# Kernel tuning notes

Measured on AMD Instinct MI355X. Metric: run time of the kernel, lower is better.

## Reference

```python
import jax, jax.numpy as jnp
import numpy as np

PI_APPROX = 3.14  # the original module uses 3.14, not math.pi
FPS = 30.0        # hard-coded sampling rate in calc_hr_torch


def setup_inputs() -> dict:
    key = jax.random.key(0)
    x = jax.random.normal(key, (4096, 4096), dtype=jnp.float32)
    return {"x": x}


def reference(x) -> jnp.ndarray:
    test_n, sig_length = x.shape
    # mean-subtract each signal (over last dim)
    x = x - jnp.mean(x, axis=-1, keepdims=True)

    # custom_fft: DFT over dim 0 (size test_n), O(N^2) via trig matmuls
    N = test_n
    n = jnp.arange(N, dtype=jnp.float32)[:, None]  # [N,1]
    k = jnp.arange(N, dtype=jnp.float32)[None, :]  # [1,N]
    ang = (-2.0 * PI_APPROX / N) * (k * n)         # [N,N]
    real_part = jnp.matmul(jnp.cos(ang), x)        # [N, sig_length]
    imag_part = jnp.matmul(jnp.sin(ang), x)

    # custom_rfft: keep non-negative frequencies along dim 0
    half = N // 2 + 1 if N % 2 == 0 else (N + 1) // 2
    real_part = real_part[:half]
    imag_part = imag_part[:half]

    Ns = sig_length
    freq = jnp.arange(Ns, dtype=jnp.float32) / (Ns / FPS)  # [sig_length]
    amplitude = jnp.sqrt(real_part ** 2 + imag_part ** 2) / Ns  # [half, sig_length]
    hr_list = freq[jnp.argmax(amplitude, axis=-1)] * 60.0       # [half]
    return hr_list
```

## Files before the change

### kernel.cpp

```cpp
#include <hip/hip_runtime.h>
#include <cmath>

typedef _Float16 f16;
typedef _Float16 f16x8 __attribute__((ext_vector_type(8)));
typedef float f32x4 __attribute__((ext_vector_type(4)));
typedef unsigned long long u64;

#define M_OUT 2049
#define NDIM 4096
#define MPAD 2112
#define CW ((float)(-2.0 * 3.14 / 4096.0))

static const size_t WS_MEAN  = 0;
static const size_t WS_CELLS = 16384;
static const size_t WS_TBL   = 40960;
static const size_t A_ELEMS  = (size_t)MPAD * NDIM;
static const size_t X_ELEMS  = (size_t)NDIM * NDIM;
static const size_t WS_XTBL  = WS_TBL + 4 * A_ELEMS * sizeof(f16);
static const size_t WS_FULL_END = WS_XTBL + 2 * X_ELEMS * sizeof(f16);
static const size_t WS_MID_END  = WS_TBL + 4 * A_ELEMS * sizeof(f16);

#define AS1 __attribute__((address_space(1)))
#define AS3 __attribute__((address_space(3)))
__device__ __forceinline__ void async_copy16(const void* gsrc, void* ldst) {
    __builtin_amdgcn_global_load_lds((const AS1 unsigned int*)gsrc,
                                     (AS3 unsigned int*)ldst, 16, 0, 0);
}

__device__ __forceinline__ void split_f16(float v, f16& hi, f16& lo) {
    hi = (f16)v;
    lo = (f16)((v - (float)hi) * 64.0f);
}

__global__ void mean_kernel(const float* __restrict__ x, float* __restrict__ meanv,
                            u64* __restrict__ cells) {
    if (blockIdx.x < 9) {
        int i = blockIdx.x * 256 + threadIdx.x;
        if (i < M_OUT) cells[i] = 0ull;
    }
    const int row = blockIdx.x;
    const float4* xr = (const float4*)(x + (size_t)row * NDIM);
    float s = 0.f;
    for (int i = threadIdx.x; i < NDIM / 4; i += 256) {
        float4 v = xr[i];
        s += (v.x + v.y) + (v.z + v.w);
    }
    for (int off = 32; off; off >>= 1) s += __shfl_down(s, off);
    __shared__ float ps[4];
    if ((threadIdx.x & 63) == 0) ps[threadIdx.x >> 6] = s;
    __syncthreads();
    if (threadIdx.x == 0) {
        float t = (ps[0] + ps[1]) + (ps[2] + ps[3]);
        meanv[row] = t * (1.0f / 4096.0f);
    }
}

__global__ __launch_bounds__(256) void nyq_partial(
    const float* __restrict__ x, const float* __restrict__ meanv,
    float* __restrict__ part)
{
    __shared__ float lc[256], ls[256];
    __shared__ float sC[128], sS[128];
    const int t = threadIdx.x;
    const int ks = blockIdx.y;
    const int kbase = ks * 256;
    sincosf(CW * (float)(2048 * (kbase + t)), &ls[t], &lc[t]);
    __syncthreads();
    const int col = blockIdx.x * 128 + (t & 127);
    const int kp  = t >> 7;
    float C = 0.f, S = 0.f;
    const float* xp = x + (size_t)(kbase + kp * 128) * NDIM + col;
    const float* mp = meanv + kbase + kp * 128;
    for (int i = 0; i < 128; ++i) {
        float v = xp[(size_t)i * NDIM] - mp[i];
        C = fmaf(lc[kp * 128 + i], v, C);
        S = fmaf(ls[kp * 128 + i], v, S);
    }
    if (kp) { sC[t - 128] = C; sS[t - 128] = S; }
    __syncthreads();
    if (!kp) {
        part[(size_t)ks * NDIM + col]            = C + sC[t];
        part[(size_t)(16 + ks) * NDIM + col]     = S + sS[t];
    }
}

__global__ __launch_bounds__(256) void nyq_reduce(
    const float* __restrict__ part, u64* __restrict__ cells)
{
    const int n = blockIdx.x * 256 + threadIdx.x;
    float C = 0.f, S = 0.f;
    for (int ks = 0; ks < 16; ++ks) {
        C += part[(size_t)ks * NDIM + n];
        S += part[(size_t)(16 + ks) * NDIM + n];
    }
    float a2 = C * C + S * S;
    u64 key = ((u64)__float_as_uint(a2) << 32) | (unsigned)(~n);
    for (int off = 1; off < 64; off <<= 1) {
        unsigned hi = (unsigned)(key >> 32), lo = (unsigned)key;
        unsigned ho = __shfl_xor(hi, off), lo2 = __shfl_xor(lo, off);
        u64 o = ((u64)ho << 32) | lo2;
        if (o > key) key = o;
    }
    if ((threadIdx.x & 63) == 0) atomicMax(cells + 2048, key);
}

__global__ void fill_tables_cm(const float* __restrict__ x, const float* __restrict__ meanv,
                               f16* __restrict__ atbl, f16* __restrict__ xtbl) {
    const int c = blockIdx.x;
    if (blockIdx.y < 9) {
        const int m = blockIdx.y * 256 + threadIdx.x;
        if (m >= MPAD) return;
        const bool valid = (m < M_OUT);
        f16x8 chv, clv, shv, slv;
        for (int j = 0; j < 8; ++j) {
            float cc = 0.f, ss = 0.f;
            if (valid) {
                int kk = c * 8 + j;
                float ang = CW * (float)(m * kk);
                sincosf(ang, &ss, &cc);
            }
            f16 h, l;
            split_f16(cc, h, l); chv[j] = h; clv[j] = l;
            split_f16(ss, h, l); shv[j] = h; slv[j] = l;
        }
        size_t idx = ((size_t)c * MPAD + m) * 8;
        *(f16x8*)(atbl + idx)                 = chv;
        *(f16x8*)(atbl + A_ELEMS + idx)       = clv;
        *(f16x8*)(atbl + 2 * A_ELEMS + idx)   = shv;
        *(f16x8*)(atbl + 3 * A_ELEMS + idx)   = slv;
    } else {
        const int n = (blockIdx.y - 9) * 256 + threadIdx.x;
        f16x8 hv, lv;
        for (int j = 0; j < 8; ++j) {
            int k = c * 8 + j;
            float v = x[(size_t)k * NDIM + n] - meanv[k];
            f16 h, l;
            split_f16(v, h, l);
            hv[j] = h; lv[j] = l;
        }
        size_t idx = ((size_t)c * NDIM + n) * 8;
        *(f16x8*)(xtbl + idx)           = hv;
        *(f16x8*)(xtbl + X_ELEMS + idx) = lv;
    }
}

__global__ __launch_bounds__(256, 2) void dft_gemm_cm(
    const f16* __restrict__ atbl, const f16* __restrict__ xtbl,
    u64* __restrict__ cells)
{
    __shared__ alignas(16) f16 sX[3][2][4][128][8];

    const int t = threadIdx.x;
    const int n0      = blockIdx.x * 128;
    const int rowBase = blockIdx.y * 64;

    const int lane = t & 63;
    const int w  = t >> 6;
    const int wm = w >> 1, wn = w & 1;
    const int q  = lane >> 4, ln = lane & 15;

    f32x4 aC0[2][4], aC1[2][4], aS0[2][4], aS1[2][4];
#pragma unroll
    for (int i = 0; i < 2; ++i)
#pragma unroll
        for (int j = 0; j < 4; ++j) {
            aC0[i][j] = (f32x4){0.f, 0.f, 0.f, 0.f};
            aC1[i][j] = (f32x4){0.f, 0.f, 0.f, 0.f};
            aS0[i][j] = (f32x4){0.f, 0.f, 0.f, 0.f};
            aS1[i][j] = (f32x4){0.f, 0.f, 0.f, 0.f};
        }

    const f16* aBase = atbl + ((size_t)q * MPAD + (rowBase + wm * 32 + ln)) * 8;

    const int xq0 = w >> 1, xh = w & 1;
    const int xq1 = xq0 + 2;
    const f16* xG0 = xtbl + ((size_t)xq0 * NDIM + n0 + xh * 64 + lane) * 8;
    const f16* xG1 = xtbl + ((size_t)xq1 * NDIM + n0 + xh * 64 + lane) * 8;
    const f16* xG2 = xG0 + X_ELEMS;
    const f16* xG3 = xG1 + X_ELEMS;

    auto loadA = [&](f16x8 (&dst)[2][4], int kc) {
#pragma unroll
        for (int tm = 0; tm < 2; ++tm)
#pragma unroll
            for (int tb = 0; tb < 4; ++tb)
                dst[tm][tb] = *(const f16x8*)(aBase + (size_t)tb * A_ELEMS
                              + ((size_t)kc * MPAD + tm * 16) * 8);
    };

    auto stageX = [&](int buf, int kc) {
        const size_t kadv = (size_t)kc * NDIM * 8;
        async_copy16(xG0 + kadv, &sX[buf][0][xq0][xh * 64][0]);
        async_copy16(xG1 + kadv, &sX[buf][0][xq1][xh * 64][0]);
        async_copy16(xG2 + kadv, &sX[buf][1][xq0][xh * 64][0]);
        async_copy16(xG3 + kadv, &sX[buf][1][xq1][xh * 64][0]);
    };

    auto compute = [&](f16x8 (&A)[2][4], int buf) {
        f16x8 bh[4], bl[4];
#pragma unroll
        for (int tn = 0; tn < 4; ++tn) {
            int nl = wn * 64 + tn * 16 + ln;
            bh[tn] = *(const f16x8*)&sX[buf][0][q][nl][0];
            bl[tn] = *(const f16x8*)&sX[buf][1][q][nl][0];
        }
        __builtin_amdgcn_s_setprio(1);
#pragma unroll
        for (int tm = 0; tm < 2; ++tm)
#pragma unroll
            for (int tn = 0; tn < 4; ++tn) {
                aC0[tm][tn] = __builtin_amdgcn_mfma_f32_16x16x32_f16(A[tm][0], bh[tn], aC0[tm][tn], 0, 0, 0);
                aC1[tm][tn] = __builtin_amdgcn_mfma_f32_16x16x32_f16(A[tm][0], bl[tn], aC1[tm][tn], 0, 0, 0);
                aC1[tm][tn] = __builtin_amdgcn_mfma_f32_16x16x32_f16(A[tm][1], bh[tn], aC1[tm][tn], 0, 0, 0);
                aS0[tm][tn] = __builtin_amdgcn_mfma_f32_16x16x32_f16(A[tm][2], bh[tn], aS0[tm][tn], 0, 0, 0);
                aS1[tm][tn] = __builtin_amdgcn_mfma_f32_16x16x32_f16(A[tm][2], bl[tn], aS1[tm][tn], 0, 0, 0);
                aS1[tm][tn] = __builtin_amdgcn_mfma_f32_16x16x32_f16(A[tm][3], bh[tn], aS1[tm][tn], 0, 0, 0);
            }
        __builtin_amdgcn_s_setprio(0);
    };

    f16x8 Aa[2][4], Ab[2][4];
    int cur = 0, nxt = 1;
    auto bump = [&]() { cur = nxt; nxt = (nxt == 2) ? 0 : nxt + 1; };

    stageX(0, 0);
    loadA(Aa, 0);

    int kc = 0;
    for (int it = 0; it < 63; ++it) {
        loadA(Ab, kc + 4);
        stageX(nxt, kc + 4);
        asm volatile("s_waitcnt vmcnt(12)" ::: "memory");
        __builtin_amdgcn_s_barrier();
        __builtin_amdgcn_sched_barrier(0);
        compute(Aa, cur);
        bump();
        kc += 4;
        loadA(Aa, kc + 4);
        stageX(nxt, kc + 4);
        asm volatile("s_waitcnt vmcnt(12)" ::: "memory");
        __builtin_amdgcn_s_barrier();
        __builtin_amdgcn_sched_barrier(0);
        compute(Ab, cur);
        bump();
        kc += 4;
    }
    loadA(Ab, kc + 4);
    stageX(nxt, kc + 4);
    asm volatile("s_waitcnt vmcnt(12)" ::: "memory");
    __builtin_amdgcn_s_barrier();
    __builtin_amdgcn_sched_barrier(0);
    compute(Aa, cur);
    bump();
    asm volatile("s_waitcnt vmcnt(0)" ::: "memory");
    __builtin_amdgcn_s_barrier();
    __builtin_amdgcn_sched_barrier(0);
    compute(Ab, cur);

    const float inv64 = 0.015625f;
#pragma unroll
    for (int tm = 0; tm < 2; ++tm) {
#pragma unroll
        for (int r = 0; r < 4; ++r) {
            u64 best = 0ull;
#pragma unroll
            for (int tn = 0; tn < 4; ++tn) {
                float C = aC0[tm][tn][r] + aC1[tm][tn][r] * inv64;
                float S = aS0[tm][tn][r] + aS1[tm][tn][r] * inv64;
                float a2 = C * C + S * S;
                int col = n0 + wn * 64 + tn * 16 + ln;
                u64 key = ((u64)__float_as_uint(a2) << 32) | (unsigned)(~col);
                if (key > best) best = key;
            }
            for (int off = 1; off < 16; off <<= 1) {
                unsigned hi = (unsigned)(best >> 32), lo = (unsigned)best;
                unsigned ho = __shfl_xor(hi, off);
                unsigned lo2 = __shfl_xor(lo, off);
                u64 o = ((u64)ho << 32) | lo2;
                if (o > best) best = o;
            }
            if (ln == 0) {
                int grow = rowBase + wm * 32 + tm * 16 + q * 4 + r;
                if (grow < M_OUT) atomicMax(cells + grow, best);
            }
        }
    }
}

__global__ void fill_tables_rm(f16* __restrict__ tbl) {
    long long g = (long long)blockIdx.x * 256 + threadIdx.x;
    if (g >= (long long)(MPAD * 512)) return;
    int m  = (int)(g >> 9);
    int kq = ((int)g & 511) * 8;
    bool valid = (m < M_OUT);
    f16x8 chv, clv, shv, slv;
    for (int j = 0; j < 8; ++j) {
        float c = 0.f, s = 0.f;
        if (valid) {
            int kk = kq + j;
            float ang = CW * (float)(m * kk);
            sincosf(ang, &s, &c);
        }
        f16 h, l;
        split_f16(c, h, l); chv[j] = h; clv[j] = l;
        split_f16(s, h, l); shv[j] = h; slv[j] = l;
    }
    size_t idx = (size_t)m * NDIM + kq;
    *(f16x8*)(tbl + idx)               = chv;
    *(f16x8*)(tbl + A_ELEMS + idx)     = clv;
    *(f16x8*)(tbl + 2 * A_ELEMS + idx) = shv;
    *(f16x8*)(tbl + 3 * A_ELEMS + idx) = slv;
}

#define PK 40
__global__ __launch_bounds__(256, 2) void dft_gemm_fb(
    const float* __restrict__ x, const float* __restrict__ meanv,
    const f16* __restrict__ tbl, int useTbl,
    u64* __restrict__ cells)
{
    __shared__ alignas(16) f16 Ach[64][PK];
    __shared__ alignas(16) f16 Acl[64][PK];
    __shared__ alignas(16) f16 Ash[64][PK];
    __shared__ alignas(16) f16 Asl[64][PK];
    __shared__ alignas(16) f16 Xh[128][PK];
    __shared__ alignas(16) f16 Xl[128][PK];

    const int t = threadIdx.x;
    const int n0      = blockIdx.x * 128;
    const int rowBase = blockIdx.y * 64;

    const int am  = t >> 2;
    const int akq = (t & 3) * 8;
    const int xn  = t & 127;
    const int xkh = (t >> 7) * 16;

    const int lane = t & 63;
    const int w  = t >> 6;
    const int wm = w >> 1, wn = w & 1;
    const int q  = lane >> 4, ln = lane & 15;

    f32x4 aC0[2][4], aC1[2][4], aS0[2][4], aS1[2][4];
    for (int i = 0; i < 2; ++i)
        for (int j = 0; j < 4; ++j) {
            aC0[i][j] = (f32x4){0.f, 0.f, 0.f, 0.f};
            aC1[i][j] = (f32x4){0.f, 0.f, 0.f, 0.f};
            aS0[i][j] = (f32x4){0.f, 0.f, 0.f, 0.f};
            aS1[i][j] = (f32x4){0.f, 0.f, 0.f, 0.f};
        }

    const int arow = rowBase + am;
    const bool avalid = (arow < M_OUT);

    for (int k0 = 0; k0 < NDIM; k0 += 32) {
        __syncthreads();
        if (useTbl) {
            size_t idx = (size_t)arow * NDIM + k0 + akq;
            *(f16x8*)&Ach[am][akq] = *(const f16x8*)(tbl + idx);
            *(f16x8*)&Acl[am][akq] = *(const f16x8*)(tbl + A_ELEMS + idx);
            *(f16x8*)&Ash[am][akq] = *(const f16x8*)(tbl + 2 * A_ELEMS + idx);
            *(f16x8*)&Asl[am][akq] = *(const f16x8*)(tbl + 3 * A_ELEMS + idx);
        } else {
            f16x8 chv, clv, shv, slv;
            for (int j = 0; j < 8; ++j) {
                float c = 0.f, s = 0.f;
                if (avalid) {
                    int kk = k0 + akq + j;
                    float ang = CW * (float)(arow * kk);
                    sincosf(ang, &s, &c);
                }
                f16 h, l;
                split_f16(c, h, l); chv[j] = h; clv[j] = l;
                split_f16(s, h, l); shv[j] = h; slv[j] = l;
            }
            *(f16x8*)&Ach[am][akq] = chv;
            *(f16x8*)&Acl[am][akq] = clv;
            *(f16x8*)&Ash[am][akq] = shv;
            *(f16x8*)&Asl[am][akq] = slv;
        }
        {
            const float* xp = x + (size_t)(k0 + xkh) * NDIM + n0 + xn;
            f16x8 h0, h1, l0, l1;
            for (int r = 0; r < 16; ++r) {
                float v = xp[(size_t)r * NDIM] - meanv[k0 + xkh + r];
                f16 hi, lo;
                split_f16(v, hi, lo);
                if (r < 8) { h0[r] = hi; l0[r] = lo; }
                else       { h1[r - 8] = hi; l1[r - 8] = lo; }
            }
            *(f16x8*)&Xh[xn][xkh]     = h0;
            *(f16x8*)&Xh[xn][xkh + 8] = h1;
            *(f16x8*)&Xl[xn][xkh]     = l0;
            *(f16x8*)&Xl[xn][xkh + 8] = l1;
        }
        __syncthreads();
        f16x8 fch[2], fcl[2], fsh[2], fsl[2], bh[4], bl[4];
        for (int tm = 0; tm < 2; ++tm) {
            int ml = wm * 32 + tm * 16 + ln;
            fch[tm] = *(const f16x8*)&Ach[ml][q * 8];
            fcl[tm] = *(const f16x8*)&Acl[ml][q * 8];
            fsh[tm] = *(const f16x8*)&Ash[ml][q * 8];
            fsl[tm] = *(const f16x8*)&Asl[ml][q * 8];
        }
        for (int tn = 0; tn < 4; ++tn) {
            int nl = wn * 64 + tn * 16 + ln;
            bh[tn] = *(const f16x8*)&Xh[nl][q * 8];
            bl[tn] = *(const f16x8*)&Xl[nl][q * 8];
        }
        for (int tm = 0; tm < 2; ++tm)
            for (int tn = 0; tn < 4; ++tn) {
                aC0[tm][tn] = __builtin_amdgcn_mfma_f32_16x16x32_f16(fch[tm], bh[tn], aC0[tm][tn], 0, 0, 0);
                aC1[tm][tn] = __builtin_amdgcn_mfma_f32_16x16x32_f16(fch[tm], bl[tn], aC1[tm][tn], 0, 0, 0);
                aC1[tm][tn] = __builtin_amdgcn_mfma_f32_16x16x32_f16(fcl[tm], bh[tn], aC1[tm][tn], 0, 0, 0);
                aS0[tm][tn] = __builtin_amdgcn_mfma_f32_16x16x32_f16(fsh[tm], bh[tn], aS0[tm][tn], 0, 0, 0);
                aS1[tm][tn] = __builtin_amdgcn_mfma_f32_16x16x32_f16(fsh[tm], bl[tn], aS1[tm][tn], 0, 0, 0);
                aS1[tm][tn] = __builtin_amdgcn_mfma_f32_16x16x32_f16(fsl[tm], bh[tn], aS1[tm][tn], 0, 0, 0);
            }
    }

    const float inv64 = 0.015625f;
    for (int tm = 0; tm < 2; ++tm) {
        for (int r = 0; r < 4; ++r) {
            u64 best = 0ull;
            for (int tn = 0; tn < 4; ++tn) {
                float C = aC0[tm][tn][r] + aC1[tm][tn][r] * inv64;
                float S = aS0[tm][tn][r] + aS1[tm][tn][r] * inv64;
                float a2 = C * C + S * S;
                int col = n0 + wn * 64 + tn * 16 + ln;
                u64 key = ((u64)__float_as_uint(a2) << 32) | (unsigned)(~col);
                if (key > best) best = key;
            }
            for (int off = 1; off < 16; off <<= 1) {
                unsigned hi = (unsigned)(best >> 32), lo = (unsigned)best;
                unsigned ho = __shfl_xor(hi, off);
                unsigned lo2 = __shfl_xor(lo, off);
                u64 o = ((u64)ho << 32) | lo2;
                if (o > best) best = o;
            }
            if (ln == 0) {
                int grow = rowBase + wm * 32 + tm * 16 + q * 4 + r;
                if (grow < M_OUT) atomicMax(cells + grow, best);
            }
        }
    }
}

__global__ void out_kernel(const u64* __restrict__ cells, float* __restrict__ out) {
    int i = blockIdx.x * 256 + threadIdx.x;
    if (i < M_OUT) {
        unsigned col = ~(unsigned)(cells[i] & 0xFFFFFFFFull);
        float freq = (float)col / (4096.0f / 30.0f);
        out[i] = freq * 60.0f;
    }
}

extern "C" void kernel_launch(void* const* d_in, const int* in_sizes, int n_in,
                              void* d_out, int out_size, void* d_ws, size_t ws_size,
                              hipStream_t stream) {
    const float* x = (const float*)d_in[0];
    char* ws = (char*)d_ws;
    float* meanv = (float*)(ws + WS_MEAN);
    u64*   cells = (u64*)(ws + WS_CELLS);
    f16*   atbl  = (f16*)(ws + WS_TBL);
    f16*   xtbl  = (f16*)(ws + WS_XTBL);
    float* nyqp  = (float*)(ws + WS_TBL);
    float* out   = (float*)d_out;

    hipLaunchKernelGGL(mean_kernel, dim3(NDIM), dim3(256), 0, stream, x, meanv, cells);

    if (ws_size >= WS_FULL_END) {
        hipLaunchKernelGGL(nyq_partial, dim3(32, 16), dim3(256), 0, stream, x, meanv, nyqp);
        hipLaunchKernelGGL(nyq_reduce, dim3(16), dim3(256), 0, stream, nyqp, cells);
        hipLaunchKernelGGL(fill_tables_cm, dim3(512, 25), dim3(256), 0, stream,
                           x, meanv, atbl, xtbl);
        hipLaunchKernelGGL(dft_gemm_cm, dim3(32, 32), dim3(256), 0, stream, atbl, xtbl, cells);
    } else if (ws_size >= WS_MID_END) {
        hipLaunchKernelGGL(fill_tables_rm, dim3(4224), dim3(256), 0, stream, atbl);
        hipLaunchKernelGGL(dft_gemm_fb, dim3(32, 33), dim3(256), 0, stream,
                           x, meanv, atbl, 1, cells);
    } else {
        hipLaunchKernelGGL(dft_gemm_fb, dim3(32, 33), dim3(256), 0, stream,
                           x, meanv, atbl, 0, cells);
    }
    hipLaunchKernelGGL(out_kernel, dim3((M_OUT + 255) / 256), dim3(256), 0, stream, cells, out);
}
```

Before: 458.0 us.

## Merge split-f16 accumulators, drop A double-buffer, raise occupancy to three waves

Stores the low f16 part of each split value unscaled, so the hi and lo MFMA products accumulate into one register set instead of two. This halves the accumulator registers. The A-fragment double buffer is removed and A is loaded just-in-time each k-step, with a tighter vmcnt wait. Launch bounds go up to three blocks per SIMD. Unscaled low parts risk precision loss, since tiny residuals can fall into f16 subnormals, and A loads are now less latency-hidden.

```diff
diff --git a/kernel.cpp b/kernel.cpp
--- a/kernel.cpp
+++ b/kernel.cpp
@@ -30,6 +30,10 @@
 __device__ __forceinline__ void split_f16(float v, f16& hi, f16& lo) {
     hi = (f16)v;
     lo = (f16)((v - (float)hi) * 64.0f);
+}
+__device__ __forceinline__ void split_raw(float v, f16& hi, f16& lo) {
+    hi = (f16)v;
+    lo = (f16)(v - (float)hi);
 }
 
 __global__ void mean_kernel(const float* __restrict__ x, float* __restrict__ meanv,
@@ -120,8 +124,8 @@
                 sincosf(ang, &ss, &cc);
             }
             f16 h, l;
-            split_f16(cc, h, l); chv[j] = h; clv[j] = l;
-            split_f16(ss, h, l); shv[j] = h; slv[j] = l;
+            split_raw(cc, h, l); chv[j] = h; clv[j] = l;
+            split_raw(ss, h, l); shv[j] = h; slv[j] = l;
         }
         size_t idx = ((size_t)c * MPAD + m) * 8;
         *(f16x8*)(atbl + idx)                 = chv;
@@ -135,7 +139,7 @@
             int k = c * 8 + j;
             float v = x[(size_t)k * NDIM + n] - meanv[k];
             f16 h, l;
-            split_f16(v, h, l);
+            split_raw(v, h, l);
             hv[j] = h; lv[j] = l;
         }
         size_t idx = ((size_t)c * NDIM + n) * 8;
@@ -144,7 +148,7 @@
     }
 }
 
-__global__ __launch_bounds__(256, 2) void dft_gemm_cm(
+__global__ __launch_bounds__(256, 3) void dft_gemm_cm(
     const f16* __restrict__ atbl, const f16* __restrict__ xtbl,
     u64* __restrict__ cells)
 {
@@ -159,15 +163,13 @@
     const int wm = w >> 1, wn = w & 1;
     const int q  = lane >> 4, ln = lane & 15;
 
-    f32x4 aC0[2][4], aC1[2][4], aS0[2][4], aS1[2][4];
+    f32x4 aC[2][4], aS[2][4];
 #pragma unroll
     for (int i = 0; i < 2; ++i)
 #pragma unroll
         for (int j = 0; j < 4; ++j) {
-            aC0[i][j] = (f32x4){0.f, 0.f, 0.f, 0.f};
-            aC1[i][j] = (f32x4){0.f, 0.f, 0.f, 0.f};
-            aS0[i][j] = (f32x4){0.f, 0.f, 0.f, 0.f};
-            aS1[i][j] = (f32x4){0.f, 0.f, 0.f, 0.f};
+            aC[i][j] = (f32x4){0.f, 0.f, 0.f, 0.f};
+            aS[i][j] = (f32x4){0.f, 0.f, 0.f, 0.f};
         }
 
     const f16* aBase = atbl + ((size_t)q * MPAD + (rowBase + wm * 32 + ln)) * 8;
@@ -209,55 +211,38 @@
         for (int tm = 0; tm < 2; ++tm)
 #pragma unroll
             for (int tn = 0; tn < 4; ++tn) {
-                aC0[tm][tn] = __builtin_amdgcn_mfma_f32_16x16x32_f16(A[tm][0], bh[tn], aC0[tm][tn], 0, 0, 0);
-                aC1[tm][tn] = __builtin_amdgcn_mfma_f32_16x16x32_f16(A[tm][0], bl[tn], aC1[tm][tn], 0, 0, 0);
-                aC1[tm][tn] = __builtin_amdgcn_mfma_f32_16x16x32_f16(A[tm][1], bh[tn], aC1[tm][tn], 0, 0, 0);
-                aS0[tm][tn] = __builtin_amdgcn_mfma_f32_16x16x32_f16(A[tm][2], bh[tn], aS0[tm][tn], 0, 0, 0);
-                aS1[tm][tn] = __builtin_amdgcn_mfma_f32_16x16x32_f16(A[tm][2], bl[tn], aS1[tm][tn], 0, 0, 0);
-                aS1[tm][tn] = __builtin_amdgcn_mfma_f32_16x16x32_f16(A[tm][3], bh[tn], aS1[tm][tn], 0, 0, 0);
+                aC[tm][tn] = __builtin_amdgcn_mfma_f32_16x16x32_f16(A[tm][0], bh[tn], aC[tm][tn], 0, 0, 0);
+                aC[tm][tn] = __builtin_amdgcn_mfma_f32_16x16x32_f16(A[tm][0], bl[tn], aC[tm][tn], 0, 0, 0);
+                aC[tm][tn] = __builtin_amdgcn_mfma_f32_16x16x32_f16(A[tm][1], bh[tn], aC[tm][tn], 0, 0, 0);
+                aS[tm][tn] = __builtin_amdgcn_mfma_f32_16x16x32_f16(A[tm][2], bh[tn], aS[tm][tn], 0, 0, 0);
+                aS[tm][tn] = __builtin_amdgcn_mfma_f32_16x16x32_f16(A[tm][2], bl[tn], aS[tm][tn], 0, 0, 0);
+                aS[tm][tn] = __builtin_amdgcn_mfma_f32_16x16x32_f16(A[tm][3], bh[tn], aS[tm][tn], 0, 0, 0);
             }
         __builtin_amdgcn_s_setprio(0);
     };
 
-    f16x8 Aa[2][4], Ab[2][4];
+    f16x8 Aa[2][4];
     int cur = 0, nxt = 1;
-    auto bump = [&]() { cur = nxt; nxt = (nxt == 2) ? 0 : nxt + 1; };
 
     stageX(0, 0);
-    loadA(Aa, 0);
-
-    int kc = 0;
-    for (int it = 0; it < 63; ++it) {
-        loadA(Ab, kc + 4);
+
+    for (int kc = 0; kc < 508; kc += 4) {
+        loadA(Aa, kc);
+        __builtin_amdgcn_sched_barrier(0);
         stageX(nxt, kc + 4);
-        asm volatile("s_waitcnt vmcnt(12)" ::: "memory");
+        __builtin_amdgcn_sched_barrier(0);
+        asm volatile("s_waitcnt vmcnt(4)" ::: "memory");
         __builtin_amdgcn_s_barrier();
         __builtin_amdgcn_sched_barrier(0);
         compute(Aa, cur);
-        bump();
-        kc += 4;
-        loadA(Aa, kc + 4);
-        stageX(nxt, kc + 4);
-        asm volatile("s_waitcnt vmcnt(12)" ::: "memory");
-        __builtin_amdgcn_s_barrier();
-        __builtin_amdgcn_sched_barrier(0);
-        compute(Ab, cur);
-        bump();
-        kc += 4;
-    }
-    loadA(Ab, kc + 4);
-    stageX(nxt, kc + 4);
-    asm volatile("s_waitcnt vmcnt(12)" ::: "memory");
+        cur = nxt; nxt = (nxt == 2) ? 0 : nxt + 1;
+    }
+    loadA(Aa, 508);
+    asm volatile("s_waitcnt vmcnt(0)" ::: "memory");
     __builtin_amdgcn_s_barrier();
     __builtin_amdgcn_sched_barrier(0);
     compute(Aa, cur);
-    bump();
-    asm volatile("s_waitcnt vmcnt(0)" ::: "memory");
-    __builtin_amdgcn_s_barrier();
-    __builtin_amdgcn_sched_barrier(0);
-    compute(Ab, cur);
-
-    const float inv64 = 0.015625f;
+
 #pragma unroll
     for (int tm = 0; tm < 2; ++tm) {
 #pragma unroll
@@ -265,8 +250,8 @@
             u64 best = 0ull;
 #pragma unroll
             for (int tn = 0; tn < 4; ++tn) {
-                float C = aC0[tm][tn][r] + aC1[tm][tn][r] * inv64;
-                float S = aS0[tm][tn][r] + aS1[tm][tn][r] * inv64;
+                float C = aC[tm][tn][r];
+                float S = aS[tm][tn][r];
                 float a2 = C * C + S * S;
                 int col = n0 + wn * 64 + tn * 16 + ln;
                 u64 key = ((u64)__float_as_uint(a2) << 32) | (unsigned)(~col);
```

Result: slower. 501.1 us (+9.4%).

## Switch DFT GEMM to 32x32x16 MFMA with unscaled split accumulation

Applied to the files above, without the earlier changes.

Replaces the 16x16x32 MFMA tiling with 32x32x16 MFMA instructions, so each wave covers its 32-row by 64-column tile with two 32x32 accumulators per component. The low-order f16 parts are no longer scaled by 64 and are summed into the same accumulator as the high parts, which halves accumulator registers and drops the recombination step in the epilogue. The aim is to cut LDS reads and register pressure and to use the larger MFMA shape. The cost is a longer 32-lane shuffle reduction per row in the epilogue, and unscaled low parts in f16 may lose precision through subnormals.

```diff
diff --git a/kernel.cpp b/kernel.cpp
--- a/kernel.cpp
+++ b/kernel.cpp
@@ -4,6 +4,7 @@
 typedef _Float16 f16;
 typedef _Float16 f16x8 __attribute__((ext_vector_type(8)));
 typedef float f32x4 __attribute__((ext_vector_type(4)));
+typedef float f32x16 __attribute__((ext_vector_type(16)));
 typedef unsigned long long u64;
 
 #define M_OUT 2049
@@ -30,6 +31,10 @@
 __device__ __forceinline__ void split_f16(float v, f16& hi, f16& lo) {
     hi = (f16)v;
     lo = (f16)((v - (float)hi) * 64.0f);
+}
+__device__ __forceinline__ void split_raw(float v, f16& hi, f16& lo) {
+    hi = (f16)v;
+    lo = (f16)(v - (float)hi);
 }
 
 __global__ void mean_kernel(const float* __restrict__ x, float* __restrict__ meanv,
@@ -120,8 +125,8 @@
                 sincosf(ang, &ss, &cc);
             }
             f16 h, l;
-            split_f16(cc, h, l); chv[j] = h; clv[j] = l;
-            split_f16(ss, h, l); shv[j] = h; slv[j] = l;
+            split_raw(cc, h, l); chv[j] = h; clv[j] = l;
+            split_raw(ss, h, l); shv[j] = h; slv[j] = l;
         }
         size_t idx = ((size_t)c * MPAD + m) * 8;
         *(f16x8*)(atbl + idx)                 = chv;
@@ -135,7 +140,7 @@
             int k = c * 8 + j;
             float v = x[(size_t)k * NDIM + n] - meanv[k];
             f16 h, l;
-            split_f16(v, h, l);
+            split_raw(v, h, l);
             hv[j] = h; lv[j] = l;
         }
         size_t idx = ((size_t)c * NDIM + n) * 8;
@@ -157,20 +162,19 @@
     const int lane = t & 63;
     const int w  = t >> 6;
     const int wm = w >> 1, wn = w & 1;
-    const int q  = lane >> 4, ln = lane & 15;
-
-    f32x4 aC0[2][4], aC1[2][4], aS0[2][4], aS1[2][4];
+    const int l31 = lane & 31;
+    const int hl  = lane >> 5;
+
+    f32x16 aC[2], aS[2];
 #pragma unroll
     for (int i = 0; i < 2; ++i)
 #pragma unroll
-        for (int j = 0; j < 4; ++j) {
-            aC0[i][j] = (f32x4){0.f, 0.f, 0.f, 0.f};
-            aC1[i][j] = (f32x4){0.f, 0.f, 0.f, 0.f};
-            aS0[i][j] = (f32x4){0.f, 0.f, 0.f, 0.f};
-            aS1[i][j] = (f32x4){0.f, 0.f, 0.f, 0.f};
-        }
-
-    const f16* aBase = atbl + ((size_t)q * MPAD + (rowBase + wm * 32 + ln)) * 8;
+        for (int j = 0; j < 16; ++j) {
+            aC[i][j] = 0.f;
+            aS[i][j] = 0.f;
+        }
+
+    const f16* aBase = atbl + ((size_t)hl * MPAD + (rowBase + wm * 32 + l31)) * 8;
 
     const int xq0 = w >> 1, xh = w & 1;
     const int xq1 = xq0 + 2;
@@ -179,13 +183,13 @@
     const f16* xG2 = xG0 + X_ELEMS;
     const f16* xG3 = xG1 + X_ELEMS;
 
-    auto loadA = [&](f16x8 (&dst)[2][4], int kc) {
-#pragma unroll
-        for (int tm = 0; tm < 2; ++tm)
-#pragma unroll
-            for (int tb = 0; tb < 4; ++tb)
-                dst[tm][tb] = *(const f16x8*)(aBase + (size_t)tb * A_ELEMS
-                              + ((size_t)kc * MPAD + tm * 16) * 8);
+    auto loadA = [&](f16x8 (&dst)[4][2], int kc) {
+#pragma unroll
+        for (int tb = 0; tb < 4; ++tb)
+#pragma unroll
+            for (int h = 0; h < 2; ++h)
+                dst[tb][h] = *(const f16x8*)(aBase + (size_t)tb * A_ELEMS
+                              + ((size_t)(kc + 2 * h) * MPAD) * 8);
     };
 
     auto stageX = [&](int buf, int kc) {
@@ -196,30 +200,27 @@
         async_copy16(xG3 + kadv, &sX[buf][1][xq1][xh * 64][0]);
     };
 
-    auto compute = [&](f16x8 (&A)[2][4], int buf) {
-        f16x8 bh[4], bl[4];
-#pragma unroll
-        for (int tn = 0; tn < 4; ++tn) {
-            int nl = wn * 64 + tn * 16 + ln;
-            bh[tn] = *(const f16x8*)&sX[buf][0][q][nl][0];
-            bl[tn] = *(const f16x8*)&sX[buf][1][q][nl][0];
-        }
+    auto compute = [&](f16x8 (&A)[4][2], int buf) {
         __builtin_amdgcn_s_setprio(1);
 #pragma unroll
-        for (int tm = 0; tm < 2; ++tm)
-#pragma unroll
-            for (int tn = 0; tn < 4; ++tn) {
-                aC0[tm][tn] = __builtin_amdgcn_mfma_f32_16x16x32_f16(A[tm][0], bh[tn], aC0[tm][tn], 0, 0, 0);
-                aC1[tm][tn] = __builtin_amdgcn_mfma_f32_16x16x32_f16(A[tm][0], bl[tn], aC1[tm][tn], 0, 0, 0);
-                aC1[tm][tn] = __builtin_amdgcn_mfma_f32_16x16x32_f16(A[tm][1], bh[tn], aC1[tm][tn], 0, 0, 0);
-                aS0[tm][tn] = __builtin_amdgcn_mfma_f32_16x16x32_f16(A[tm][2], bh[tn], aS0[tm][tn], 0, 0, 0);
-                aS1[tm][tn] = __builtin_amdgcn_mfma_f32_16x16x32_f16(A[tm][2], bl[tn], aS1[tm][tn], 0, 0, 0);
-                aS1[tm][tn] = __builtin_amdgcn_mfma_f32_16x16x32_f16(A[tm][3], bh[tn], aS1[tm][tn], 0, 0, 0);
-            }
+        for (int tn2 = 0; tn2 < 2; ++tn2) {
+            const int nl = wn * 64 + tn2 * 32 + l31;
+#pragma unroll
+            for (int h = 0; h < 2; ++h) {
+                f16x8 bh = *(const f16x8*)&sX[buf][0][2 * h + hl][nl][0];
+                f16x8 bl = *(const f16x8*)&sX[buf][1][2 * h + hl][nl][0];
+                aC[tn2] = __builtin_amdgcn_mfma_f32_32x32x16_f16(A[0][h], bh, aC[tn2], 0, 0, 0);
+                aC[tn2] = __builtin_amdgcn_mfma_f32_32x32x16_f16(A[0][h], bl, aC[tn2], 0, 0, 0);
+                aC[tn2] = __builtin_amdgcn_mfma_f32_32x32x16_f16(A[1][h], bh, aC[tn2], 0, 0, 0);
+                aS[tn2] = __builtin_amdgcn_mfma_f32_32x32x16_f16(A[2][h], bh, aS[tn2], 0, 0, 0);
+                aS[tn2] = __builtin_amdgcn_mfma_f32_32x32x16_f16(A[2][h], bl, aS[tn2], 0, 0, 0);
+                aS[tn2] = __builtin_amdgcn_mfma_f32_32x32x16_f16(A[3][h], bh, aS[tn2], 0, 0, 0);
+            }
+        }
         __builtin_amdgcn_s_setprio(0);
     };
 
-    f16x8 Aa[2][4], Ab[2][4];
+    f16x8 Aa[4][2], Ab[4][2];
     int cur = 0, nxt = 1;
     auto bump = [&]() { cur = nxt; nxt = (nxt == 2) ? 0 : nxt + 1; };
 
@@ -257,31 +258,26 @@
     __builtin_amdgcn_sched_barrier(0);
     compute(Ab, cur);
 
-    const float inv64 = 0.015625f;
-#pragma unroll
-    for (int tm = 0; tm < 2; ++tm) {
-#pragma unroll
-        for (int r = 0; r < 4; ++r) {
-            u64 best = 0ull;
-#pragma unroll
-            for (int tn = 0; tn < 4; ++tn) {
-                float C = aC0[tm][tn][r] + aC1[tm][tn][r] * inv64;
-                float S = aS0[tm][tn][r] + aS1[tm][tn][r] * inv64;
-                float a2 = C * C + S * S;
-                int col = n0 + wn * 64 + tn * 16 + ln;
-                u64 key = ((u64)__float_as_uint(a2) << 32) | (unsigned)(~col);
-                if (key > best) best = key;
-            }
-            for (int off = 1; off < 16; off <<= 1) {
-                unsigned hi = (unsigned)(best >> 32), lo = (unsigned)best;
+#pragma unroll
+    for (int tn2 = 0; tn2 < 2; ++tn2) {
+        const int col = n0 + wn * 64 + tn2 * 32 + l31;
+#pragma unroll
+        for (int r = 0; r < 16; ++r) {
+            float C = aC[tn2][r];
+            float S = aS[tn2][r];
+            float a2 = C * C + S * S;
+            u64 key = ((u64)__float_as_uint(a2) << 32) | (unsigned)(~col);
+#pragma unroll
+            for (int off = 1; off < 32; off <<= 1) {
+                unsigned hi = (unsigned)(key >> 32), lo = (unsigned)key;
                 unsigned ho = __shfl_xor(hi, off);
                 unsigned lo2 = __shfl_xor(lo, off);
                 u64 o = ((u64)ho << 32) | lo2;
-                if (o > best) best = o;
-            }
-            if (ln == 0) {
-                int grow = rowBase + wm * 32 + tm * 16 + q * 4 + r;
-                if (grow < M_OUT) atomicMax(cells + grow, best);
+                if (o > key) key = o;
+            }
+            if (l31 == 0) {
+                int grow = rowBase + wm * 32 + (r & 3) + 8 * (r >> 2) + 4 * hl;
+                if (grow < M_OUT) atomicMax(cells + grow, key);
             }
         }
     }
```

Measured after the change: 540.7 us. 18.0% more time.
